# Kernel optimization log

Measured on AMD Instinct MI355X. Metric: run time of the kernel, lower is better.

## Reference

```python
import jax, jax.numpy as jnp
import numpy as np

D, B, E, O = 16, 8, 2048, 2048  # delays, batch, pre, post


def setup_inputs() -> dict:
    key = jax.random.key(0)
    k1, k2, k3, k4, k5, k6 = jax.random.split(key, 6)
    # Sparse nonnegative connectivity scaled by wmax (here wmax=1)
    conn = (jax.random.uniform(k1, (E, O)) < 0.2).astype(jnp.float32)
    W = jax.random.uniform(k2, (E, O), dtype=jnp.float32) * conn
    # align_signs: per-presynaptic-neuron sign in {-1,+1}, zeroed where W<=0
    signs_pre = jnp.where(jax.random.uniform(k3, (E,)) < 0.8, 1.0, -1.0)
    signs = jnp.where(W > 0, signs_pre[:, None], 0.0).astype(jnp.float32)
    Xd = (jax.random.uniform(k4, (D, B, E)) < 0.05).astype(jnp.float32)
    # STP module output (before the +1 applied in forward)
    Wshort = 0.1 * jax.random.normal(k5, (D, B, E), dtype=jnp.float32)
    # delaymap: binary routing mask (delay, pre, post)
    delaymap = (jax.random.uniform(k6, (D, E, O)) < 0.3).astype(jnp.float32)
    return {"W": W, "signs": signs, "Xd": Xd, "Wshort": Wshort, "delaymap": delaymap}


def reference(W, signs, Xd, Wshort, delaymap):
    # DeltaSynapse.forward, active, has_STDP=False, has_STP=True:
    #   W_eff = signs * W                      (e, o)
    #   Wshort_mod = shortterm(Xd) + 1         (d, b, e)
    #   I = einsum('eo,dbe,deo,dbe->bo', W_eff, Xd, delaymap, Wshort_mod)
    Weff = signs * W
    I = jnp.einsum('eo,dbe,deo,dbe->bo', Weff, Xd, delaymap, Wshort + 1.0)
    return I
```

## Files before the change

kernel.cpp:

```cpp
#include <hip/hip_runtime.h>
#include <cstdint>
#include <cstddef>

#define DD 16
#define BB 8
#define EE 2048
#define OO 2048
#define NCH 256

__global__ void pack_coeffs(const float* __restrict__ Xd,
                            const float* __restrict__ Ws,
                            float* __restrict__ Cpack,
                            unsigned* __restrict__ mask,
                            float* __restrict__ out) {
    int i = blockIdx.x * 256 + threadIdx.x;
    if (i < BB * OO) out[i] = 0.0f;
    if (i >= DD * BB * EE) return;
    int e  = i & (EE - 1);
    int db = i >> 11;
    int d  = db >> 3;
    int b  = db & 7;
    float x = Xd[i];
    float v = x * (Ws[i] + 1.0f);
    Cpack[((size_t)e * DD + d) * BB + b] = v;
    if (v != 0.0f) atomicOr(&mask[e], 1u << d);
}

__device__ __forceinline__ void fma4(float4& a, const float4& x, float s) {
    a.x = fmaf(x.x, s, a.x);
    a.y = fmaf(x.y, s, a.y);
    a.z = fmaf(x.z, s, a.z);
    a.w = fmaf(x.w, s, a.w);
}

__global__ __launch_bounds__(256, 4)
void synapse_main(const float* __restrict__ W,
                  const float* __restrict__ S,
                  const float* __restrict__ DM,
                  const float* __restrict__ Cpack,
                  const unsigned* __restrict__ mask,
                  float* __restrict__ out) {
    const int ot   = blockIdx.x;
    const int ch   = blockIdx.y;
    const int wave = threadIdx.x >> 6;
    const int lane = threadIdx.x & 63;
    const int o0   = ot * 256 + lane * 4;
    const int e0   = ch * 8 + wave * 2;
    const int e1   = e0 + 1;

    float4 acc[BB];
#pragma unroll
    for (int b = 0; b < BB; ++b) acc[b] = make_float4(0.f, 0.f, 0.f, 0.f);

    float4 w0 = *reinterpret_cast<const float4*>(W + (size_t)e0 * OO + o0);
    float4 s0 = *reinterpret_cast<const float4*>(S + (size_t)e0 * OO + o0);
    float4 w1 = *reinterpret_cast<const float4*>(W + (size_t)e1 * OO + o0);
    float4 s1 = *reinterpret_cast<const float4*>(S + (size_t)e1 * OO + o0);
    float4 wf0, wf1;
    wf0.x = w0.x * s0.x; wf0.y = w0.y * s0.y;
    wf0.z = w0.z * s0.z; wf0.w = w0.w * s0.w;
    wf1.x = w1.x * s1.x; wf1.y = w1.y * s1.y;
    wf1.z = w1.z * s1.z; wf1.w = w1.w * s1.w;

    unsigned m0 = mask[e0];
    unsigned m1 = mask[e1];

    while (m0 | m1) {
        const unsigned a0 = m0, a1 = m1;
        float4 c00, c01, dm0;
        float4 c10, c11, dm1;
        if (a0) {
            const int d = __builtin_ctz(m0);
            m0 &= (m0 - 1);
            const float4* cp = reinterpret_cast<const float4*>(
                Cpack + ((size_t)e0 * DD + d) * BB);
            c00 = cp[0];
            c01 = cp[1];
            dm0 = *reinterpret_cast<const float4*>(
                DM + ((size_t)d * EE + e0) * OO + o0);
        }
        if (a1) {
            const int d = __builtin_ctz(m1);
            m1 &= (m1 - 1);
            const float4* cp = reinterpret_cast<const float4*>(
                Cpack + ((size_t)e1 * DD + d) * BB);
            c10 = cp[0];
            c11 = cp[1];
            dm1 = *reinterpret_cast<const float4*>(
                DM + ((size_t)d * EE + e1) * OO + o0);
        }
        if (a0) {
            float4 dw;
            dw.x = dm0.x * wf0.x; dw.y = dm0.y * wf0.y;
            dw.z = dm0.z * wf0.z; dw.w = dm0.w * wf0.w;
            fma4(acc[0], dw, c00.x); fma4(acc[1], dw, c00.y);
            fma4(acc[2], dw, c00.z); fma4(acc[3], dw, c00.w);
            fma4(acc[4], dw, c01.x); fma4(acc[5], dw, c01.y);
            fma4(acc[6], dw, c01.z); fma4(acc[7], dw, c01.w);
        }
        if (a1) {
            float4 dw;
            dw.x = dm1.x * wf1.x; dw.y = dm1.y * wf1.y;
            dw.z = dm1.z * wf1.z; dw.w = dm1.w * wf1.w;
            fma4(acc[0], dw, c10.x); fma4(acc[1], dw, c10.y);
            fma4(acc[2], dw, c10.z); fma4(acc[3], dw, c10.w);
            fma4(acc[4], dw, c11.x); fma4(acc[5], dw, c11.y);
            fma4(acc[6], dw, c11.z); fma4(acc[7], dw, c11.w);
        }
    }

    __shared__ __align__(16) float red[4][4][256];
    const int t = threadIdx.x;
#pragma unroll
    for (int p = 0; p < 2; ++p) {
#pragma unroll
        for (int bb = 0; bb < 4; ++bb)
            *reinterpret_cast<float4*>(&red[wave][bb][lane * 4]) = acc[p * 4 + bb];
        __syncthreads();
#pragma unroll
        for (int bb = 0; bb < 4; ++bb) {
            float s = red[0][bb][t] + red[1][bb][t] +
                      red[2][bb][t] + red[3][bb][t];
            atomicAdd(out + (size_t)(p * 4 + bb) * OO + ot * 256 + t, s);
        }
        __syncthreads();
    }
}

__global__ __launch_bounds__(256, 4)
void synapse_nows(const float* __restrict__ W,
                  const float* __restrict__ S,
                  const float* __restrict__ Xd,
                  const float* __restrict__ Ws,
                  const float* __restrict__ DM,
                  float* __restrict__ out) {
    const int ot   = blockIdx.x;
    const int ch   = blockIdx.y;
    const int wave = threadIdx.x >> 6;
    const int lane = threadIdx.x & 63;
    const int o0   = ot * 256 + lane * 4;

    float4 acc[BB];
#pragma unroll
    for (int b = 0; b < BB; ++b) acc[b] = make_float4(0.f, 0.f, 0.f, 0.f);

#pragma unroll
    for (int ei = 0; ei < 2; ++ei) {
        const int e = ch * 8 + wave * 2 + ei;

        float4 w4 = *reinterpret_cast<const float4*>(W + (size_t)e * OO + o0);
        float4 s4 = *reinterpret_cast<const float4*>(S + (size_t)e * OO + o0);
        float4 wf;
        wf.x = w4.x * s4.x; wf.y = w4.y * s4.y;
        wf.z = w4.z * s4.z; wf.w = w4.w * s4.w;

        for (int d = 0; d < DD; ++d) {
            float c[BB];
            bool nz = false;
#pragma unroll
            for (int b = 0; b < BB; ++b) {
                size_t idx = (size_t)(d * BB + b) * EE + e;
                float x = Xd[idx];
                c[b] = x * (Ws[idx] + 1.0f);
                nz |= (c[b] != 0.f);
            }
            if (!nz) continue;
            float4 dm = *reinterpret_cast<const float4*>(
                DM + ((size_t)d * EE + e) * OO + o0);
            float4 dw;
            dw.x = dm.x * wf.x; dw.y = dm.y * wf.y;
            dw.z = dm.z * wf.z; dw.w = dm.w * wf.w;
#pragma unroll
            for (int b = 0; b < BB; ++b) fma4(acc[b], dw, c[b]);
        }
    }

    __shared__ __align__(16) float red[4][4][256];
    const int t = threadIdx.x;
#pragma unroll
    for (int p = 0; p < 2; ++p) {
#pragma unroll
        for (int bb = 0; bb < 4; ++bb)
            *reinterpret_cast<float4*>(&red[wave][bb][lane * 4]) = acc[p * 4 + bb];
        __syncthreads();
#pragma unroll
        for (int bb = 0; bb < 4; ++bb) {
            float s = red[0][bb][t] + red[1][bb][t] +
                      red[2][bb][t] + red[3][bb][t];
            atomicAdd(out + (size_t)(p * 4 + bb) * OO + ot * 256 + t, s);
        }
        __syncthreads();
    }
}

__global__ void zero_out(float* __restrict__ out) {
    int i = blockIdx.x * 256 + threadIdx.x;
    if (i < BB * OO) out[i] = 0.0f;
}

extern "C" void kernel_launch(void* const* d_in, const int* in_sizes, int n_in,
                              void* d_out, int out_size, void* d_ws, size_t ws_size,
                              hipStream_t stream) {
    const float* W  = (const float*)d_in[0];
    const float* S  = (const float*)d_in[1];
    const float* Xd = (const float*)d_in[2];
    const float* Ws = (const float*)d_in[3];
    const float* DM = (const float*)d_in[4];
    float* out = (float*)d_out;

    const size_t packBytes = (size_t)EE * DD * BB * sizeof(float);
    const size_t maskBytes = (size_t)EE * sizeof(unsigned);

    char* ws = (char*)d_ws;
    const bool canPack = ws_size >= packBytes + maskBytes;

    dim3 grid(8, NCH), blk(256);

    if (canPack) {
        float*    Cp = (float*)ws;
        unsigned* mk = (unsigned*)(ws + packBytes);
        hipMemsetAsync(mk, 0, maskBytes, stream);
        pack_coeffs<<<(DD * BB * EE + 255) / 256, 256, 0, stream>>>(Xd, Ws, Cp, mk, out);
        synapse_main<<<grid, blk, 0, stream>>>(W, S, DM, Cp, mk, out);
    } else {
        zero_out<<<(BB * OO + 255) / 256, 256, 0, stream>>>(out);
        synapse_nows<<<grid, blk, 0, stream>>>(W, S, Xd, Ws, DM, out);
    }
}
```

Baseline: 353.1 us.

## Build delay masks in-kernel via ballot, drop atomic mask and memset, 4 pre-neurons per wave

The global per-presynaptic delay bitmask built with atomicOr, and its memset, are removed. Each wave now loads the packed coefficient rows for its four presynaptic neurons, with one lane per (neuron, delay), and derives the nonzero-delay masks with a wave ballot. Coefficients are then broadcast with shuffles instead of being reloaded from memory. Each wave covers four neurons instead of two and the grid's chunk count is halved, which trades fewer launches and atomics for more work and more in-flight delaymap loads per block.

```diff
diff --git a/kernel.cpp b/kernel.cpp
--- a/kernel.cpp
+++ b/kernel.cpp
@@ -6,12 +6,11 @@
 #define BB 8
 #define EE 2048
 #define OO 2048
-#define NCH 256
+#define NCH 128
 
 __global__ void pack_coeffs(const float* __restrict__ Xd,
                             const float* __restrict__ Ws,
                             float* __restrict__ Cpack,
-                            unsigned* __restrict__ mask,
                             float* __restrict__ out) {
     int i = blockIdx.x * 256 + threadIdx.x;
     if (i < BB * OO) out[i] = 0.0f;
@@ -21,9 +20,7 @@
     int d  = db >> 3;
     int b  = db & 7;
     float x = Xd[i];
-    float v = x * (Ws[i] + 1.0f);
-    Cpack[((size_t)e * DD + d) * BB + b] = v;
-    if (v != 0.0f) atomicOr(&mask[e], 1u << d);
+    Cpack[(size_t)e * (DD * BB) + d * BB + b] = x * (Ws[i] + 1.0f);
 }
 
 __device__ __forceinline__ void fma4(float4& a, const float4& x, float s) {
@@ -38,74 +35,71 @@
                   const float* __restrict__ S,
                   const float* __restrict__ DM,
                   const float* __restrict__ Cpack,
-                  const unsigned* __restrict__ mask,
                   float* __restrict__ out) {
-    const int ot   = blockIdx.x;
-    const int ch   = blockIdx.y;
-    const int wave = threadIdx.x >> 6;
-    const int lane = threadIdx.x & 63;
-    const int o0   = ot * 256 + lane * 4;
-    const int e0   = ch * 8 + wave * 2;
-    const int e1   = e0 + 1;
+    const int ot    = blockIdx.x;
+    const int ch    = blockIdx.y;
+    const int wave  = threadIdx.x >> 6;
+    const int lane  = threadIdx.x & 63;
+    const int o0    = ot * 256 + lane * 4;
+    const int ebase = ch * 16 + wave * 4;
+
+    const int q_ln = lane >> 4;
+    const int d_ln = lane & 15;
+    const float4* crow = reinterpret_cast<const float4*>(
+        Cpack + ((size_t)(ebase + q_ln) * (DD * BB)) + d_ln * BB);
+    float4 ca = crow[0];
+    float4 cb = crow[1];
+    bool nz = (ca.x != 0.f) | (ca.y != 0.f) | (ca.z != 0.f) | (ca.w != 0.f) |
+              (cb.x != 0.f) | (cb.y != 0.f) | (cb.z != 0.f) | (cb.w != 0.f);
+    unsigned long long bal = __ballot(nz);
+    unsigned m[4];
+#pragma unroll
+    for (int q = 0; q < 4; ++q) m[q] = (unsigned)(bal >> (16 * q)) & 0xFFFFu;
+
+    float4 wf[4];
+#pragma unroll
+    for (int q = 0; q < 4; ++q) {
+        float4 w4 = *reinterpret_cast<const float4*>(W + (size_t)(ebase + q) * OO + o0);
+        float4 s4 = *reinterpret_cast<const float4*>(S + (size_t)(ebase + q) * OO + o0);
+        wf[q].x = w4.x * s4.x; wf[q].y = w4.y * s4.y;
+        wf[q].z = w4.z * s4.z; wf[q].w = w4.w * s4.w;
+    }
 
     float4 acc[BB];
 #pragma unroll
     for (int b = 0; b < BB; ++b) acc[b] = make_float4(0.f, 0.f, 0.f, 0.f);
 
-    float4 w0 = *reinterpret_cast<const float4*>(W + (size_t)e0 * OO + o0);
-    float4 s0 = *reinterpret_cast<const float4*>(S + (size_t)e0 * OO + o0);
-    float4 w1 = *reinterpret_cast<const float4*>(W + (size_t)e1 * OO + o0);
-    float4 s1 = *reinterpret_cast<const float4*>(S + (size_t)e1 * OO + o0);
-    float4 wf0, wf1;
-    wf0.x = w0.x * s0.x; wf0.y = w0.y * s0.y;
-    wf0.z = w0.z * s0.z; wf0.w = w0.w * s0.w;
-    wf1.x = w1.x * s1.x; wf1.y = w1.y * s1.y;
-    wf1.z = w1.z * s1.z; wf1.w = w1.w * s1.w;
-
-    unsigned m0 = mask[e0];
-    unsigned m1 = mask[e1];
-
-    while (m0 | m1) {
-        const unsigned a0 = m0, a1 = m1;
-        float4 c00, c01, dm0;
-        float4 c10, c11, dm1;
-        if (a0) {
-            const int d = __builtin_ctz(m0);
-            m0 &= (m0 - 1);
-            const float4* cp = reinterpret_cast<const float4*>(
-                Cpack + ((size_t)e0 * DD + d) * BB);
-            c00 = cp[0];
-            c01 = cp[1];
-            dm0 = *reinterpret_cast<const float4*>(
-                DM + ((size_t)d * EE + e0) * OO + o0);
-        }
-        if (a1) {
-            const int d = __builtin_ctz(m1);
-            m1 &= (m1 - 1);
-            const float4* cp = reinterpret_cast<const float4*>(
-                Cpack + ((size_t)e1 * DD + d) * BB);
-            c10 = cp[0];
-            c11 = cp[1];
-            dm1 = *reinterpret_cast<const float4*>(
-                DM + ((size_t)d * EE + e1) * OO + o0);
-        }
-        if (a0) {
-            float4 dw;
-            dw.x = dm0.x * wf0.x; dw.y = dm0.y * wf0.y;
-            dw.z = dm0.z * wf0.z; dw.w = dm0.w * wf0.w;
-            fma4(acc[0], dw, c00.x); fma4(acc[1], dw, c00.y);
-            fma4(acc[2], dw, c00.z); fma4(acc[3], dw, c00.w);
-            fma4(acc[4], dw, c01.x); fma4(acc[5], dw, c01.y);
-            fma4(acc[6], dw, c01.z); fma4(acc[7], dw, c01.w);
-        }
-        if (a1) {
-            float4 dw;
-            dw.x = dm1.x * wf1.x; dw.y = dm1.y * wf1.y;
-            dw.z = dm1.z * wf1.z; dw.w = dm1.w * wf1.w;
-            fma4(acc[0], dw, c10.x); fma4(acc[1], dw, c10.y);
-            fma4(acc[2], dw, c10.z); fma4(acc[3], dw, c10.w);
-            fma4(acc[4], dw, c11.x); fma4(acc[5], dw, c11.y);
-            fma4(acc[6], dw, c11.z); fma4(acc[7], dw, c11.w);
+    while (m[0] | m[1] | m[2] | m[3]) {
+        float4 dmv[4];
+        int    dsrc[4];
+        unsigned act = 0;
+#pragma unroll
+        for (int q = 0; q < 4; ++q) {
+            if (m[q]) {
+                const int d = __builtin_ctz(m[q]);
+                m[q] &= (m[q] - 1);
+                dsrc[q] = q * 16 + d;
+                dmv[q] = *reinterpret_cast<const float4*>(
+                    DM + ((size_t)d * EE + (ebase + q)) * OO + o0);
+                act |= 1u << q;
+            }
+        }
+#pragma unroll
+        for (int q = 0; q < 4; ++q) {
+            if (act & (1u << q)) {
+                const int sl = dsrc[q];
+                float4 dw;
+                dw.x = dmv[q].x * wf[q].x; dw.y = dmv[q].y * wf[q].y;
+                dw.z = dmv[q].z * wf[q].z; dw.w = dmv[q].w * wf[q].w;
+                fma4(acc[0], dw, __shfl(ca.x, sl));
+                fma4(acc[1], dw, __shfl(ca.y, sl));
+                fma4(acc[2], dw, __shfl(ca.z, sl));
+                fma4(acc[3], dw, __shfl(ca.w, sl));
+                fma4(acc[4], dw, __shfl(cb.x, sl));
+                fma4(acc[5], dw, __shfl(cb.y, sl));
+                fma4(acc[6], dw, __shfl(cb.z, sl));
+                fma4(acc[7], dw, __shfl(cb.w, sl));
+            }
         }
     }
 
@@ -134,20 +128,19 @@
                   const float* __restrict__ Ws,
                   const float* __restrict__ DM,
                   float* __restrict__ out) {
-    const int ot   = blockIdx.x;
-    const int ch   = blockIdx.y;
-    const int wave = threadIdx.x >> 6;
-    const int lane = threadIdx.x & 63;
-    const int o0   = ot * 256 + lane * 4;
+    const int ot    = blockIdx.x;
+    const int ch    = blockIdx.y;
+    const int wave  = threadIdx.x >> 6;
+    const int lane  = threadIdx.x & 63;
+    const int o0    = ot * 256 + lane * 4;
+    const int ebase = ch * 16 + wave * 4;
 
     float4 acc[BB];
 #pragma unroll
     for (int b = 0; b < BB; ++b) acc[b] = make_float4(0.f, 0.f, 0.f, 0.f);
 
-#pragma unroll
-    for (int ei = 0; ei < 2; ++ei) {
-        const int e = ch * 8 + wave * 2 + ei;
-
+    for (int ei = 0; ei < 4; ++ei) {
+        const int e = ebase + ei;
         float4 w4 = *reinterpret_cast<const float4*>(W + (size_t)e * OO + o0);
         float4 s4 = *reinterpret_cast<const float4*>(S + (size_t)e * OO + o0);
         float4 wf;
@@ -209,19 +202,13 @@
     float* out = (float*)d_out;
 
     const size_t packBytes = (size_t)EE * DD * BB * sizeof(float);
-    const size_t maskBytes = (size_t)EE * sizeof(unsigned);
-
-    char* ws = (char*)d_ws;
-    const bool canPack = ws_size >= packBytes + maskBytes;
 
     dim3 grid(8, NCH), blk(256);
 
-    if (canPack) {
-        float*    Cp = (float*)ws;
-        unsigned* mk = (unsigned*)(ws + packBytes);
-        hipMemsetAsync(mk, 0, maskBytes, stream);
-        pack_coeffs<<<(DD * BB * EE + 255) / 256, 256, 0, stream>>>(Xd, Ws, Cp, mk, out);
-        synapse_main<<<grid, blk, 0, stream>>>(W, S, DM, Cp, mk, out);
+    if (ws_size >= packBytes) {
+        float* Cp = (float*)d_ws;
+        pack_coeffs<<<(DD * BB * EE + 255) / 256, 256, 0, stream>>>(Xd, Ws, Cp, out);
+        synapse_main<<<grid, blk, 0, stream>>>(W, S, DM, Cp, out);
     } else {
         zero_out<<<(BB * OO + 255) / 256, 256, 0, stream>>>(out);
         synapse_nows<<<grid, blk, 0, stream>>>(W, S, Xd, Ws, DM, out);
```

New measurement: 349.3 us. Within noise of the previous version (-1.1%).
